# Performance work log

Measured on AMD Instinct MI355X. Metric: run time of the kernel, lower is better.

The kernel has to match this reference:

```python
import jax, jax.numpy as jnp
import numpy as np

# dims
B, L = 2, 1024            # batch, seq len (queries == keys)
DQ, DK, DSRC = 1024, 1024, 512
VIEWS, WIDTH, TOPK = 8, 4, 8
DVP = DQ // VIEWS         # per-view head dim = 128
PAD_F = (WIDTH - 1) // 2  # dilocal 'same' zero padding (stride=1, dilation=1)
PAD_B = (WIDTH - 1) - PAD_F


def setup_inputs() -> dict:
    key = jax.random.key(0)
    ks = jax.random.split(key, 5)
    s = 0.02
    return {
        "query": jax.random.normal(ks[0], (B, L, DQ), jnp.float32),
        "key_t": jax.random.normal(ks[1], (B, L, DK), jnp.float32),
        "source": jax.random.normal(ks[2], (B, L, DSRC), jnp.float32),
        "wq": jax.random.normal(ks[3], (VIEWS, DVP, DQ), jnp.float32) * s,
        "bq": jnp.zeros((VIEWS, DVP), jnp.float32),
        "wk": jax.random.normal(ks[4], (VIEWS, DVP, DK), jnp.float32) * s,
        "bk": jnp.zeros((VIEWS, DVP), jnp.float32),
    }


def reference(query, key_t, source, wq, bq, wk, bk):
    # --- ViewPointFactory.forward ---
    # multi-view projections: [B, L, D] -> [B, views, L, dvp]
    q = jnp.einsum('bld,vkd->bvlk', query, wq) + bq[None, :, None, :]
    k = jnp.einsum('bld,vkd->bvlk', key_t, wk) + bk[None, :, None, :]
    # attention scores over all keys: [B, views, Lq, Lk] (no sqrt(d) scaling in source)
    score = jnp.einsum('bvqd,bvkd->bvqk', q, k)
    # torch.sort(descending) + slice == top_k with sorted values
    vals, idx = jax.lax.top_k(score, TOPK)          # [B, views, Lq, TOPK]
    weights = jax.nn.softmax(vals, axis=-1)

    # --- ViewPoint.__call__(source) ---
    # dilocal: width-WIDTH local windows, stride 1, dilation 1, zero 'same' pad
    padded = jnp.pad(source, ((0, 0), (PAD_F, PAD_B), (0, 0)))
    win_idx = jnp.arange(L)[:, None] + jnp.arange(WIDTH)[None, :]  # [L, WIDTH]
    windows = padded[:, win_idx, :]                 # [B, L, WIDTH, DSRC]

    # gather the top-k key windows per (view, query): [B, views, Lq, TOPK, WIDTH, DSRC]
    gathered = jax.vmap(lambda w, i: w[i])(windows, idx)
    # weighted sum over top-k -> [B, views, Lq, WIDTH, DSRC]
    out = jnp.einsum('bvqk,bvqkwd->bvqwd', weights, gathered)
    return out
```

## Files before the change

### kernel.cpp

```cpp
#include <hip/hip_runtime.h>
#include <cstdint>

#define L_SEQ 1024
#define DSRC 512
#define XPL 2097152L
#define WPL 1048576L

typedef __attribute__((ext_vector_type(8))) short short8;
typedef __attribute__((ext_vector_type(4))) float floatx4;

__device__ __forceinline__ unsigned short f2bf(float f) {
  unsigned int x = __float_as_uint(f);
  x += 0x7fff + ((x >> 16) & 1);
  return (unsigned short)(x >> 16);
}
__device__ __forceinline__ float bf2f(unsigned short h) {
  return __uint_as_float((unsigned)h << 16);
}
__device__ __forceinline__ void split3(float f, unsigned short* h) {
  h[0] = f2bf(f);
  float d = f - bf2f(h[0]);
  h[1] = f2bf(d);
  h[2] = f2bf(d - bf2f(h[1]));
}

__device__ __forceinline__ void gload_lds16(const void* g, void* l) {
  __builtin_amdgcn_global_load_lds(
      (const __attribute__((address_space(1))) unsigned int*)g,
      (__attribute__((address_space(3))) unsigned int*)l, 16, 0, 0);
}

__device__ __forceinline__ bool better(float av, int ac, float bv, int bc) {
  return av > bv || (av == bv && ac < bc);
}
__device__ __forceinline__ void ins8f(float (&tv)[8], int (&ti)[8], float v, int c) {
  if (v > tv[7]) {
    tv[7] = v; ti[7] = c;
#pragma unroll
    for (int s = 7; s > 0; s--) {
      float x = tv[s], y = tv[s - 1];
      int xi = ti[s], yi = ti[s - 1];
      bool sw = x > y;
      tv[s] = sw ? y : x;     tv[s - 1] = sw ? x : y;
      ti[s] = sw ? yi : xi;   ti[s - 1] = sw ? xi : yi;
    }
  }
}
__device__ __forceinline__ void quadmerge_store(float (&tv)[8], int (&ti)[8],
                                                float* Mv, int* Mi, int base, int quad) {
#pragma unroll
  for (int t = 0; t < 8; t++) {
    float bv = tv[0]; int bc = ti[0];
    float ov = __shfl_xor(bv, 16); int oc = __shfl_xor(bc, 16);
    if (better(ov, oc, bv, bc)) { bv = ov; bc = oc; }
    ov = __shfl_xor(bv, 32); oc = __shfl_xor(bc, 32);
    if (better(ov, oc, bv, bc)) { bv = ov; bc = oc; }
    if (bc == ti[0]) {
#pragma unroll
      for (int s = 0; s < 7; s++) { tv[s] = tv[s + 1]; ti[s] = ti[s + 1]; }
      tv[7] = -1e30f; ti[7] = 0x7FFFFFFF;
    }
    if (quad == 0) { Mv[base + t] = bv; Mi[base + t] = bc; }
  }
}

__global__ __launch_bounds__(256) void split_inputs_k(
    const float* __restrict__ query, const float* __restrict__ key_t,
    const float* __restrict__ wq, const float* __restrict__ wk,
    ushort* __restrict__ xs, ushort* __restrict__ wsp) {
  int blk = blockIdx.x;
  const float* in; ushort* out; long pl; int idx;
  if (blk < 2048)      { in = query; out = xs;           pl = XPL; idx = blk; }
  else if (blk < 4096) { in = key_t; out = xs + 3 * XPL; pl = XPL; idx = blk - 2048; }
  else if (blk < 5120) { in = wq;    out = wsp;          pl = WPL; idx = blk - 4096; }
  else                 { in = wk;    out = wsp + 3 * WPL; pl = WPL; idx = blk - 5120; }
  long e = (long)idx * 1024 + threadIdx.x * 4;
  float4 v = *(const float4*)(in + e);
  unsigned short h0[3], h1[3], h2[3], h3[3];
  split3(v.x, h0); split3(v.y, h1); split3(v.z, h2); split3(v.w, h3);
#pragma unroll
  for (int s = 0; s < 3; s++) {
    ushort4 u; u.x = h0[s]; u.y = h1[s]; u.z = h2[s]; u.w = h3[s];
    *(ushort4*)(out + s * pl + e) = u;
  }
}

__global__ __launch_bounds__(512, 2) void proj_gemm_k(
    const ushort* __restrict__ xs, const ushort* __restrict__ wsp,
    ushort* __restrict__ qs, ushort* __restrict__ ks,
    const float* __restrict__ bq, const float* __restrict__ bk) {
  __shared__ ushort As[2][3][4096];
  __shared__ ushort Bs[2][3][4096];
  int z = blockIdx.z;
  const ushort* Ab = xs + (long)z * 3 * XPL + (long)blockIdx.y * 128 * 1024;
  const ushort* Bb = wsp + (long)z * 3 * WPL + (long)blockIdx.x * 128 * 1024;

  int tid = threadIdx.x;
  int lane = tid & 63, wv = tid >> 6;
  int wm = wv >> 2, wn = wv & 3;
  int quad = lane >> 4, l16 = lane & 15;

  int sr = tid >> 2;
  int scq = (((tid & 3) ^ ((sr >> 1) & 3)) << 3);

  floatx4 acc[4][2] = {};

#pragma unroll
  for (int s = 0; s < 3; s++) {
    gload_lds16(Ab + (long)s * XPL + (long)sr * 1024 + scq, &As[0][s][wv * 512]);
    gload_lds16(Bb + (long)s * WPL + (long)sr * 1024 + scq, &Bs[0][s][wv * 512]);
  }
  __syncthreads();

  int cur = 0;
#pragma unroll 2
  for (int t = 0; t < 32; t++) {
    if (t < 31) {
      int k0 = (t + 1) * 32;
#pragma unroll
      for (int s = 0; s < 3; s++) {
        gload_lds16(Ab + (long)s * XPL + (long)sr * 1024 + k0 + scq, &As[cur ^ 1][s][wv * 512]);
        gload_lds16(Bb + (long)s * WPL + (long)sr * 1024 + k0 + scq, &Bs[cur ^ 1][s][wv * 512]);
      }
    }
    short8 af[3][4];
#pragma unroll
    for (int s = 0; s < 3; s++)
#pragma unroll
      for (int i = 0; i < 4; i++) {
        int row = wm * 64 + i * 16 + l16;
        int qa = (quad ^ ((row >> 1) & 3)) << 3;
        af[s][i] = *(const short8*)(&As[cur][s][row * 32 + qa]);
      }
#pragma unroll
    for (int j = 0; j < 2; j++) {
      int rowb = wn * 32 + j * 16 + l16;
      int boff = rowb * 32 + ((quad ^ ((rowb >> 1) & 3)) << 3);
      short8 b0 = *(const short8*)(&Bs[cur][0][boff]);
      short8 b1 = *(const short8*)(&Bs[cur][1][boff]);
      short8 b2 = *(const short8*)(&Bs[cur][2][boff]);
#pragma unroll
      for (int i = 0; i < 4; i++) {
        acc[i][j] = __builtin_amdgcn_mfma_f32_16x16x32_bf16(af[1][i], b1, acc[i][j], 0, 0, 0);
        acc[i][j] = __builtin_amdgcn_mfma_f32_16x16x32_bf16(af[0][i], b2, acc[i][j], 0, 0, 0);
        acc[i][j] = __builtin_amdgcn_mfma_f32_16x16x32_bf16(af[2][i], b0, acc[i][j], 0, 0, 0);
        acc[i][j] = __builtin_amdgcn_mfma_f32_16x16x32_bf16(af[0][i], b1, acc[i][j], 0, 0, 0);
        acc[i][j] = __builtin_amdgcn_mfma_f32_16x16x32_bf16(af[1][i], b0, acc[i][j], 0, 0, 0);
        acc[i][j] = __builtin_amdgcn_mfma_f32_16x16x32_bf16(af[0][i], b0, acc[i][j], 0, 0, 0);
      }
    }
    __syncthreads();
    cur ^= 1;
  }

  ushort* Ob = z ? ks : qs;
  const float* bias = z ? bk : bq;
#pragma unroll
  for (int j = 0; j < 2; j++) {
    int col = blockIdx.x * 128 + wn * 32 + j * 16 + l16;
    float bv = bias[col];
#pragma unroll
    for (int i = 0; i < 4; i++) {
#pragma unroll
      for (int r = 0; r < 4; r++) {
        long row = blockIdx.y * 128 + wm * 64 + i * 16 + quad * 4 + r;
        float val = acc[i][j][r] + bv;
        unsigned short h[3]; split3(val, h);
        long e = row * 1024 + col;
#pragma unroll
        for (int s = 0; s < 3; s++) Ob[s * XPL + e] = h[s];
      }
    }
  }
}

__global__ __launch_bounds__(512, 4) void score_topk_k(
    const ushort* __restrict__ qs, const ushort* __restrict__ ks,
    float* __restrict__ wts, int* __restrict__ idxs) {
  __shared__ __align__(16) ushort smem[36864];
  ushort* Qsm = smem;
  ushort* Kb0 = smem + 12288;
  float* Mv = (float*)(smem + 12288);
  int*   Mi = (int*)(smem + 12288 + 4096);

  int fid = blockIdx.x + 32 * (blockIdx.y + 8 * blockIdx.z);
  int xcd = fid & 7, jj = fid >> 3;
  int pair = xcd * 2 + (jj & 1);
  int rt = jj >> 1;
  int v = pair & 7, b = pair >> 3;

  const long arow0 = (long)b * 1024 + rt * 32;
  const long brow0 = (long)b * 1024;
  const int vb = v * 128;

  int tid = threadIdx.x;
  int lane = tid & 63, wv = tid >> 6;
  int kg = wv & 3, qg = wv >> 2;
  int quad = lane >> 4, l16 = lane & 15;

#pragma unroll
  for (int n = 0; n < 3; n++) {
    int base = n * 512 + wv * 64;
    int sl = base + lane;
    int s = sl >> 9, rem = sl & 511;
    int r = rem >> 4, sq = rem & 15;
    int qb = sq ^ (r & 7);
    gload_lds16(qs + (long)s * XPL + (arow0 + r) * 1024 + vb + qb * 8,
                &Qsm[base * 8]);
  }

  const ushort* gKp[3]; int ldsKo[3];
#pragma unroll
  for (int n = 0; n < 3; n++) {
    int base = n * 512 + wv * 64;
    int sl = base + lane;
    int s = sl >> 9, rem = sl & 511;
    int c = rem >> 2, sq = rem & 3;
    int qb = sq ^ ((c >> 1) & 3);
    gKp[n] = ks + (long)s * XPL + (brow0 + c) * 1024 + vb + qb * 8;
    ldsKo[n] = base * 8;
  }
  auto stageK = [&](int step, int bsel) {
    long off = (long)(step >> 2) * 131072 + (step & 3) * 32;
    ushort* Kd = Kb0 + bsel * 12288;
#pragma unroll
    for (int n = 0; n < 3; n++)
      gload_lds16(gKp[n] + off, &Kd[ldsKo[n]]);
  };

  stageK(0, 0);
  __syncthreads();

  floatx4 acc[2] = {};
  float tv[8]; int ti[8];
#pragma unroll
  for (int t = 0; t < 8; t++) { tv[t] = -1e30f; ti[t] = 0x7FFFFFFF; }
  float pend[8];
  int pbase = 0;

  int buf = 0;
  for (int ct = 0; ct < 8; ct++) {
#pragma unroll
    for (int kk = 0; kk < 4; kk++) {
      int step = ct * 4 + kk;
      if (step < 31) stageK(step + 1, buf ^ 1);

      const ushort* Kc = Kb0 + buf * 12288;
      short8 qf[3], kf[3][2];
#pragma unroll
      for (int s = 0; s < 3; s++) {
        int q = qg * 16 + l16;
        int sqa = (kk * 4 + quad) ^ (q & 7);
        qf[s] = *(const short8*)(&Qsm[s * 4096 + q * 128 + sqa * 8]);
      }
#pragma unroll
      for (int s = 0; s < 3; s++)
#pragma unroll
        for (int i = 0; i < 2; i++) {
          int c = kg * 32 + i * 16 + l16;
          int sqb = quad ^ ((c >> 1) & 3);
          kf[s][i] = *(const short8*)(&Kc[s * 4096 + c * 32 + sqb * 8]);
        }
#pragma unroll
      for (int i = 0; i < 2; i++) {
        acc[i] = __builtin_amdgcn_mfma_f32_16x16x32_bf16(kf[1][i], qf[1], acc[i], 0, 0, 0);
        acc[i] = __builtin_amdgcn_mfma_f32_16x16x32_bf16(kf[2][i], qf[0], acc[i], 0, 0, 0);
        acc[i] = __builtin_amdgcn_mfma_f32_16x16x32_bf16(kf[0][i], qf[2], acc[i], 0, 0, 0);
        acc[i] = __builtin_amdgcn_mfma_f32_16x16x32_bf16(kf[1][i], qf[0], acc[i], 0, 0, 0);
        acc[i] = __builtin_amdgcn_mfma_f32_16x16x32_bf16(kf[0][i], qf[1], acc[i], 0, 0, 0);
        acc[i] = __builtin_amdgcn_mfma_f32_16x16x32_bf16(kf[0][i], qf[0], acc[i], 0, 0, 0);
      }

      if (ct > 0) {
        const int t0 = kk * 2, t1 = kk * 2 + 1;
        ins8f(tv, ti, pend[t0], pbase + ((t0 >> 2) << 4) + (quad << 2) + (t0 & 3));
        ins8f(tv, ti, pend[t1], pbase + ((t1 >> 2) << 4) + (quad << 2) + (t1 & 3));
      }
      __syncthreads();
      buf ^= 1;
    }
#pragma unroll
    for (int i = 0; i < 2; i++)
#pragma unroll
      for (int r = 0; r < 4; r++) {
        pend[i * 4 + r] = acc[i][r];
        acc[i][r] = 0.0f;
      }
    pbase = ct * 128 + kg * 32;
  }
#pragma unroll
  for (int t = 0; t < 8; t++)
    ins8f(tv, ti, pend[t], pbase + ((t >> 2) << 4) + (quad << 2) + (t & 3));

  int row = qg * 16 + l16;
  quadmerge_store(tv, ti, Mv, Mi, (kg * 32 + row) * 8, quad);
  __syncthreads();

  if (tid < 32) {
    int q = tid;
    int i0 = 0, i1 = 0, i2 = 0, i3 = 0;
    float pv[8]; int pc[8];
#pragma unroll
    for (int t = 0; t < 8; t++) {
      float v0 = Mv[(0 * 32 + q) * 8 + i0]; int c0 = Mi[(0 * 32 + q) * 8 + i0];
      float v1 = Mv[(1 * 32 + q) * 8 + i1]; int c1 = Mi[(1 * 32 + q) * 8 + i1];
      float v2 = Mv[(2 * 32 + q) * 8 + i2]; int c2 = Mi[(2 * 32 + q) * 8 + i2];
      float v3 = Mv[(3 * 32 + q) * 8 + i3]; int c3 = Mi[(3 * 32 + q) * 8 + i3];
      bool b01 = better(v1, c1, v0, c0);
      float w01v = b01 ? v1 : v0; int w01c = b01 ? c1 : c0; int w01l = b01 ? 1 : 0;
      bool b23 = better(v3, c3, v2, c2);
      float w23v = b23 ? v3 : v2; int w23c = b23 ? c3 : c2; int w23l = b23 ? 3 : 2;
      bool bf_ = better(w23v, w23c, w01v, w01c);
      float wvv = bf_ ? w23v : w01v; int wcc = bf_ ? w23c : w01c;
      int wl = bf_ ? w23l : w01l;
      i0 += (wl == 0); i1 += (wl == 1); i2 += (wl == 2); i3 += (wl == 3);
      pv[t] = wvv; pc[t] = wcc;
    }
    float m = pv[0], sum = 0.f, e[8];
#pragma unroll
    for (int t = 0; t < 8; t++) { e[t] = __expf(pv[t] - m); sum += e[t]; }
    float inv = 1.0f / sum;
    long grow = (long)b * 8192 + v * 1024 + rt * 32 + q;
#pragma unroll
    for (int t = 0; t < 8; t++) {
      wts[grow * 8 + t] = e[t] * inv;
      idxs[grow * 8 + t] = pc[t];
    }
  }
}

__global__ __launch_bounds__(256) void gather_out_k(const float* __restrict__ src,
                                                    const float* __restrict__ wts,
                                                    const int* __restrict__ idxs,
                                                    float* __restrict__ out) {
  int rowid = blockIdx.x;
  int b = rowid >> 13;
  int tid = threadIdx.x;
  int d4 = tid & 127;
  int w0 = (tid >> 7) << 1;
  const float4* s4 = (const float4*)src + (long)b * (L_SEQ * (DSRC / 4));
  float wt[8]; int id[8];
#pragma unroll
  for (int k = 0; k < 8; k++) {
    wt[k] = wts[(long)rowid * 8 + k];
    id[k] = idxs[(long)rowid * 8 + k];
  }
  float ax = 0, ay = 0, az = 0, aw = 0;
  float bx = 0, by = 0, bz2 = 0, bw = 0;
#pragma unroll
  for (int k = 0; k < 8; k++) {
    int r0 = id[k] + w0 - 1;
    if ((unsigned)r0 < (unsigned)L_SEQ) {
      float4 x = s4[(long)r0 * 128 + d4];
      ax += wt[k] * x.x; ay += wt[k] * x.y; az += wt[k] * x.z; aw += wt[k] * x.w;
    }
    int r1 = r0 + 1;
    if ((unsigned)r1 < (unsigned)L_SEQ) {
      float4 x = s4[(long)r1 * 128 + d4];
      bx += wt[k] * x.x; by += wt[k] * x.y; bz2 += wt[k] * x.z; bw += wt[k] * x.w;
    }
  }
  float4* o4 = (float4*)out + ((long)rowid * 4 + w0) * 128 + d4;
  o4[0] = make_float4(ax, ay, az, aw);
  o4[128] = make_float4(bx, by, bz2, bw);
}

extern "C" void kernel_launch(void* const* d_in, const int* in_sizes, int n_in,
                              void* d_out, int out_size, void* d_ws, size_t ws_size,
                              hipStream_t stream) {
  (void)in_sizes; (void)n_in; (void)out_size; (void)ws_size;
  const float* query  = (const float*)d_in[0];
  const float* key_t  = (const float*)d_in[1];
  const float* source = (const float*)d_in[2];
  const float* wq     = (const float*)d_in[3];
  const float* bq     = (const float*)d_in[4];
  const float* wk     = (const float*)d_in[5];
  const float* bk     = (const float*)d_in[6];

  char* ws = (char*)d_ws;
  ushort* qs  = (ushort*)(ws);
  ushort* ksp = (ushort*)(ws + 12582912);
  float*  wts = (float*)(ws + 25165824);
  int*    idxs= (int*)(ws + 25690112);
  ushort* xs  = (ushort*)(ws + 26214400);
  ushort* wsp = (ushort*)(ws + 51380224);

  split_inputs_k<<<6144, 256, 0, stream>>>(query, key_t, wq, wk, xs, wsp);
  proj_gemm_k<<<dim3(8, 16, 2), 512, 0, stream>>>(xs, wsp, qs, ksp, bq, bk);
  score_topk_k<<<dim3(32, 8, 2), 512, 0, stream>>>(qs, ksp, wts, idxs);
  gather_out_k<<<16384, 256, 0, stream>>>(source, wts, idxs, (float*)d_out);
}
```

Baseline: 289.8 us.

## Fuse top-k gather and weighted sum into score kernel epilogue

Drops the separate gather kernel. The score/top-k kernel now keeps the softmax weights and indices in shared memory and computes the weighted window sum straight into the output. This removes a kernel launch and the global round trip of weights and indices. In exchange, the 512-block score kernel must now write the whole 64 MB output with fewer blocks than the old 16384-block gather launch, so memory-level parallelism for the bandwidth-bound output stage may drop.

```diff
diff --git a/kernel.cpp b/kernel.cpp
--- a/kernel.cpp
+++ b/kernel.cpp
@@ -176,12 +176,14 @@
 
 __global__ __launch_bounds__(512, 4) void score_topk_k(
     const ushort* __restrict__ qs, const ushort* __restrict__ ks,
-    float* __restrict__ wts, int* __restrict__ idxs) {
+    const float* __restrict__ src, float* __restrict__ out) {
   __shared__ __align__(16) ushort smem[36864];
   ushort* Qsm = smem;
   ushort* Kb0 = smem + 12288;
   float* Mv = (float*)(smem + 12288);
   int*   Mi = (int*)(smem + 12288 + 4096);
+  float* Fw = (float*)smem;
+  int*   Fi = (int*)(smem + 2048);
 
   int fid = blockIdx.x + 32 * (blockIdx.y + 8 * blockIdx.z);
   int xcd = fid & 7, jj = fid >> 3;
@@ -320,49 +322,49 @@
 #pragma unroll
     for (int t = 0; t < 8; t++) { e[t] = __expf(pv[t] - m); sum += e[t]; }
     float inv = 1.0f / sum;
-    long grow = (long)b * 8192 + v * 1024 + rt * 32 + q;
 #pragma unroll
     for (int t = 0; t < 8; t++) {
-      wts[grow * 8 + t] = e[t] * inv;
-      idxs[grow * 8 + t] = pc[t];
-    }
-  }
-}
-
-__global__ __launch_bounds__(256) void gather_out_k(const float* __restrict__ src,
-                                                    const float* __restrict__ wts,
-                                                    const int* __restrict__ idxs,
-                                                    float* __restrict__ out) {
-  int rowid = blockIdx.x;
-  int b = rowid >> 13;
-  int tid = threadIdx.x;
-  int d4 = tid & 127;
-  int w0 = (tid >> 7) << 1;
-  const float4* s4 = (const float4*)src + (long)b * (L_SEQ * (DSRC / 4));
-  float wt[8]; int id[8];
-#pragma unroll
-  for (int k = 0; k < 8; k++) {
-    wt[k] = wts[(long)rowid * 8 + k];
-    id[k] = idxs[(long)rowid * 8 + k];
-  }
-  float ax = 0, ay = 0, az = 0, aw = 0;
-  float bx = 0, by = 0, bz2 = 0, bw = 0;
-#pragma unroll
-  for (int k = 0; k < 8; k++) {
-    int r0 = id[k] + w0 - 1;
-    if ((unsigned)r0 < (unsigned)L_SEQ) {
-      float4 x = s4[(long)r0 * 128 + d4];
-      ax += wt[k] * x.x; ay += wt[k] * x.y; az += wt[k] * x.z; aw += wt[k] * x.w;
-    }
-    int r1 = r0 + 1;
-    if ((unsigned)r1 < (unsigned)L_SEQ) {
-      float4 x = s4[(long)r1 * 128 + d4];
-      bx += wt[k] * x.x; by += wt[k] * x.y; bz2 += wt[k] * x.z; bw += wt[k] * x.w;
-    }
-  }
-  float4* o4 = (float4*)out + ((long)rowid * 4 + w0) * 128 + d4;
-  o4[0] = make_float4(ax, ay, az, aw);
-  o4[128] = make_float4(bx, by, bz2, bw);
+      Fw[q * 8 + t] = e[t] * inv;
+      Fi[q * 8 + t] = pc[t];
+    }
+  }
+  __syncthreads();
+
+  {
+    int q = tid >> 4, t16 = tid & 15;
+    int w0 = (t16 >> 3) << 1;
+    int dl = t16 & 7;
+    float wt[8]; int id[8];
+#pragma unroll
+    for (int k = 0; k < 8; k++) {
+      wt[k] = Fw[q * 8 + k];
+      id[k] = Fi[q * 8 + k];
+    }
+    const float4* s4 = (const float4*)src + (long)b * (L_SEQ * (DSRC / 4));
+    long rowid = (long)b * 8192 + v * 1024 + rt * 32 + q;
+    float4* o4 = (float4*)out + ((long)rowid * 4 + w0) * 128;
+#pragma unroll
+    for (int m = 0; m < 16; m++) {
+      int d4 = m * 8 + dl;
+      float ax = 0, ay = 0, az = 0, aw = 0;
+      float bx = 0, by = 0, bz2 = 0, bw = 0;
+#pragma unroll
+      for (int k = 0; k < 8; k++) {
+        int r0 = id[k] + w0 - 1;
+        if ((unsigned)r0 < (unsigned)L_SEQ) {
+          float4 x = s4[(long)r0 * 128 + d4];
+          ax += wt[k] * x.x; ay += wt[k] * x.y; az += wt[k] * x.z; aw += wt[k] * x.w;
+        }
+        int r1 = r0 + 1;
+        if ((unsigned)r1 < (unsigned)L_SEQ) {
+          float4 x = s4[(long)r1 * 128 + d4];
+          bx += wt[k] * x.x; by += wt[k] * x.y; bz2 += wt[k] * x.z; bw += wt[k] * x.w;
+        }
+      }
+      o4[d4] = make_float4(ax, ay, az, aw);
+      o4[128 + d4] = make_float4(bx, by, bz2, bw);
+    }
+  }
 }
 
 extern "C" void kernel_launch(void* const* d_in, const int* in_sizes, int n_in,
@@ -380,13 +382,10 @@
   char* ws = (char*)d_ws;
   ushort* qs  = (ushort*)(ws);
   ushort* ksp = (ushort*)(ws + 12582912);
-  float*  wts = (float*)(ws + 25165824);
-  int*    idxs= (int*)(ws + 25690112);
-  ushort* xs  = (ushort*)(ws + 26214400);
-  ushort* wsp = (ushort*)(ws + 51380224);
+  ushort* xs  = (ushort*)(ws + 25165824);
+  ushort* wsp = (ushort*)(ws + 50331648);
 
   split_inputs_k<<<6144, 256, 0, stream>>>(query, key_t, wq, wk, xs, wsp);
   proj_gemm_k<<<dim3(8, 16, 2), 512, 0, stream>>>(xs, wsp, qs, ksp, bq, bk);
-  score_topk_k<<<dim3(32, 8, 2), 512, 0, stream>>>(qs, ksp, wts, idxs);
-  gather_out_k<<<16384, 256, 0, stream>>>(source, wts, idxs, (float*)d_out);
-}
+  score_topk_k<<<dim3(32, 8, 2), 512, 0, stream>>>(qs, ksp, source, (float*)d_out);
+}
```

Measured after the change: 297.7 us. 2.7% more time.
